# Kernel optimization log

Measured on AMD Instinct MI355X. Metric: run time of the kernel, lower is better.

The kernel has to match this reference:

```python
import jax, jax.numpy as jnp
import numpy as np

B, N, D = 32, 2048, 1024


def setup_inputs() -> dict:
    key = jax.random.key(0)
    k1, k2, k3, k4, k5, k6 = jax.random.split(key, 6)
    encoded = jax.random.normal(k1, (B, N, D), dtype=jnp.float32)
    decoder_state = jax.random.normal(k2, (B, D), dtype=jnp.float32)
    mask = jax.random.randint(k3, (B, N), 0, 2, dtype=jnp.int32)
    scale = 1.0 / np.sqrt(D)
    W1 = jax.random.normal(k4, (D, D), dtype=jnp.float32) * scale  # applied as x @ W1
    W2 = jax.random.normal(k5, (D, D), dtype=jnp.float32) * scale
    vt = jax.random.normal(k6, (D,), dtype=jnp.float32) * scale
    return {"encoded": encoded, "decoder_state": decoder_state, "mask": mask,
            "W1": W1, "W2": W2, "vt": vt}


def reference(encoded, decoder_state, mask, W1, W2, vt):
    temperature = 1.0
    # process_encoded: W1(encoded)  [B, N, D]
    enc = jnp.einsum('bnd,de->bne', encoded, W1)
    # W2(decoder_state)  [B, D] -> broadcast-add over N
    dec = decoder_state @ W2
    # vt(tanh(.)).squeeze(2)  -> logits [B, N]
    u = jnp.einsum('bnd,d->bn', jnp.tanh(enc + dec[:, None, :]), vt)
    # masked log-softmax with temperature over dim=1
    logits = u / temperature + jnp.log(mask.astype(u.dtype) + 1e-45)
    return jax.nn.log_softmax(logits, axis=1)
```

## Files before the change

### kernel.cpp

```cpp
#include <hip/hip_runtime.h>

typedef _Float16 half8 __attribute__((ext_vector_type(8)));
typedef __fp16   pk2   __attribute__((ext_vector_type(2)));
typedef float    f32x4 __attribute__((ext_vector_type(4)));

#define GLOBAL_AS __attribute__((address_space(1)))
#define LDS_AS    __attribute__((address_space(3)))

static constexpr int Bb = 32;
static constexpr int Nn = 2048;
static constexpr int Dd = 1024;
static constexpr int M  = Bb * Nn;


__global__ void prep_w1(const float* __restrict__ W1, _Float16* __restrict__ W1TT) {
    int g = blockIdx.x * 256 + threadIdx.x;
    int chunk = g >> 10;
    int u = g & 1023;
    int q = u >> 7, sc = u & 127;
    int cl = sc ^ (2 * (q & 3));
    int et = chunk >> 5, t = (chunk >> 1) & 15, h = chunk & 1;
    int e  = et * 256 + h * 128 + cl;
    int k0 = t * 64 + q * 8;
    half8 hh;
#pragma unroll
    for (int j = 0; j < 8; ++j)
        hh[j] = (_Float16)W1[(size_t)(k0 + j) * Dd + e];
    *(half8*)(W1TT + (size_t)g * 8) = hh;
}

__global__ void prep_enc(const float* __restrict__ A, _Float16* __restrict__ A_p) {
    __shared__ _Float16 T[128 * 64];
    const int c = blockIdx.x;
    const int tid = threadIdx.x;
    const int mtile = c >> 5, t = (c >> 1) & 15, h = c & 1;
    const int r = tid >> 1, kh = tid & 1;
    const float* src = A + (size_t)(mtile * 256 + h * 128 + r) * Dd + t * 64 + kh * 32;
    const int rx = r & 7;
#pragma unroll
    for (int i = 0; i < 4; ++i) {
        f32x4 a  = *(const f32x4*)(src + i * 8);
        f32x4 b2 = *(const f32x4*)(src + i * 8 + 4);
        half8 hh; pk2 p;
        p = __builtin_amdgcn_cvt_pkrtz(a.x, a.y);   hh[0] = p[0]; hh[1] = p[1];
        p = __builtin_amdgcn_cvt_pkrtz(a.z, a.w);   hh[2] = p[0]; hh[3] = p[1];
        p = __builtin_amdgcn_cvt_pkrtz(b2.x, b2.y); hh[4] = p[0]; hh[5] = p[1];
        p = __builtin_amdgcn_cvt_pkrtz(b2.z, b2.w); hh[6] = p[0]; hh[7] = p[1];
        *(half8*)(T + r * 64 + (((kh * 4 + i) ^ rx) * 8)) = hh;
    }
    __syncthreads();
    const size_t cb = (size_t)c * 8192;
#pragma unroll
    for (int i = 0; i < 4; ++i) {
        int u = i * 256 + tid;
        int q = u >> 7, sr = u & 127;
        int lr = sr ^ (2 * (q & 3));
        half8 hh = *(const half8*)(T + lr * 64 + ((q ^ (lr & 7)) * 8));
        *(half8*)(A_p + cb + (size_t)u * 8) = hh;
    }
}

__global__ void dec_kernel(const float* __restrict__ ds, const float* __restrict__ W2,
                           float* __restrict__ dec) {
    __shared__ float part[4][64];
    int b = blockIdx.x, ech = blockIdx.y;
    int tid = threadIdx.x;
    int e = ech * 64 + (tid & 63);
    int dc = tid >> 6;
    float acc = 0.f;
#pragma unroll 4
    for (int d = dc * 256; d < dc * 256 + 256; ++d)
        acc += ds[b * Dd + d] * W2[(size_t)d * Dd + e];
    part[dc][tid & 63] = acc;
    __syncthreads();
    if (tid < 64)
        dec[b * Dd + e] = part[0][tid] + part[1][tid] + part[2][tid] + part[3][tid];
}

#define BAR     asm volatile("s_barrier" ::: "memory")
#define LGKM(n) asm volatile("s_waitcnt lgkmcnt(" #n ")" ::: "memory")
#define VM(n)   asm volatile("s_waitcnt vmcnt(" #n ")" ::: "memory")

#define RD_A(dst, base) do { _Pragma("unroll") \
  for (int ks = 0; ks < 2; ++ks) { const int qb = ((ks * 4 + qq) * 128) * 8; \
    _Pragma("unroll") for (int m2 = 0; m2 < 4; ++m2) \
      dst[m2][ks] = *(const half8*)&lds[(base) + qb + (m2 * 32 + rA) * 8]; } } while (0)

#define RD_B(dst, base) do { _Pragma("unroll") \
  for (int ks = 0; ks < 2; ++ks) { const int qb = ((ks * 4 + qq) * 128) * 8; \
    _Pragma("unroll") for (int j2 = 0; j2 < 2; ++j2) \
      dst[j2][ks] = *(const half8*)&lds[(base) + qb + (j2 * 64 + rB) * 8]; } } while (0)

#define MFMAQ(A_, B_, ro, co) do { __builtin_amdgcn_s_setprio(1); \
  _Pragma("unroll") for (int m2 = 0; m2 < 4; ++m2) \
  _Pragma("unroll") for (int j2 = 0; j2 < 2; ++j2) { \
    acc[(ro) + m2][(co) + j2] = __builtin_amdgcn_mfma_f32_16x16x32_f16( \
        A_[m2][0], B_[j2][0], acc[(ro) + m2][(co) + j2], 0, 0, 0); \
    acc[(ro) + m2][(co) + j2] = __builtin_amdgcn_mfma_f32_16x16x32_f16( \
        A_[m2][1], B_[j2][1], acc[(ro) + m2][(co) + j2], 0, 0, 0); } \
  __builtin_amdgcn_s_setprio(0); } while (0)

__global__ __launch_bounds__(512) void gemm8(
    const _Float16* __restrict__ A_p, const _Float16* __restrict__ W1TT,
    const float* __restrict__ dec, const float* __restrict__ vt,
    float* __restrict__ u_part)
{
    extern __shared__ _Float16 lds[];

    const int g  = blockIdx.x;
    const int wg = (g & 7) * 128 + (g >> 3);
    const int et    = wg & 3;
    const int mtile = wg >> 2;

    const int tid  = threadIdx.x;
    const int lane = tid & 63, wid = tid >> 6;
    const int wr = wid >> 2, wc = wid & 3;
    const int qq = lane >> 4, l15 = lane & 15;
    const int l15s = l15 ^ (2 * qq);
    const int rA = wr * 16 + l15s;
    const int rB = wc * 16 + l15s;

    f32x4 acc[8][4] = {};
    half8 a0[4][2], a1[4][2], b0[2][2], b1[2][2];

    const size_t abase = (size_t)mtile * 32 * 8192;
    const size_t bbase = (size_t)et * 32 * 8192;
    const int uoff = tid * 8;

    auto stA = [&](int t2, int h) {
        const _Float16* gp = A_p + abase + ((size_t)(t2 * 2 + h) << 13) + uoff;
        _Float16* lp = lds + ((((t2 & 1) * 2 + h) << 13) + (wid << 9));
        __builtin_amdgcn_global_load_lds((const GLOBAL_AS void*)gp,
                                         (LDS_AS void*)lp, 16, 0, 0);
        __builtin_amdgcn_global_load_lds((const GLOBAL_AS void*)(gp + 4096),
                                         (LDS_AS void*)(lp + 4096), 16, 0, 0);
    };
    auto stB = [&](int t2, int h) {
        const _Float16* gp = W1TT + bbase + ((size_t)(t2 * 2 + h) << 13) + uoff;
        _Float16* lp = lds + (32768 + (((t2 & 1) * 2 + h) << 13) + (wid << 9));
        __builtin_amdgcn_global_load_lds((const GLOBAL_AS void*)gp,
                                         (LDS_AS void*)lp, 16, 0, 0);
        __builtin_amdgcn_global_load_lds((const GLOBAL_AS void*)(gp + 4096),
                                         (LDS_AS void*)(lp + 4096), 16, 0, 0);
    };

    stA(0, 0); stB(0, 1); stA(0, 1); stB(0, 0); stA(1, 0); stB(1, 1);
    VM(4);
    BAR;
    RD_A(a0, 0);
    RD_B(b0, 32768);

#pragma unroll 1
    for (int i = 0; i < 8; ++i) {
        const int E = 2 * i, O = E + 1;
        const bool nl = (i < 7);

        RD_B(b1, 32768 + 8192);
        stA(O, 1);
        BAR; LGKM(4);
        MFMAQ(a0, b0, 0, 0);
        BAR;

        RD_A(a1, 8192);
        stB(O, 0);
        BAR; LGKM(8);
        MFMAQ(a0, b1, 0, 2);
        VM(6);
        BAR;

        RD_A(a0, 16384);
        if (nl) stA(E + 2, 0);
        BAR; LGKM(8);
        MFMAQ(a1, b1, 4, 2);
        BAR;

        if (nl) { stB(E + 2, 1); VM(4); }
        else    { VM(0); }
        BAR;
        MFMAQ(a1, b0, 4, 0);
        RD_B(b0, 32768 + 16384);
        BAR;

        RD_B(b1, 32768 + 16384 + 8192);
        if (nl) stA(E + 2, 1);
        BAR; LGKM(4);
        MFMAQ(a0, b0, 0, 0);
        BAR;

        RD_A(a1, 16384 + 8192);
        if (nl) stB(E + 2, 0);
        BAR; LGKM(8);
        MFMAQ(a0, b1, 0, 2);
        VM(6);
        BAR;

        if (nl) { RD_A(a0, 0);
                  stA(O + 2, 0); }
        BAR;
        if (nl) { LGKM(8); } else { LGKM(0); }
        MFMAQ(a1, b1, 4, 2);
        BAR;

        if (nl) stB(O + 2, 1);
        VM(4);
        BAR;
        MFMAQ(a1, b0, 4, 0);
        if (nl) RD_B(b0, 32768);
        BAR;
    }

    const int b = mtile >> 3;
    float vtv[4], dcv[4];
#pragma unroll
    for (int nf = 0; nf < 4; ++nf) {
        int e = et * 256 + (nf >> 1) * 128 + (nf & 1) * 64 + wc * 16 + l15;
        vtv[nf] = vt[e];
        dcv[nf] = dec[b * Dd + e];
    }
    float* usum = (float*)lds;
#pragma unroll
    for (int hm = 0; hm < 8; ++hm) {
        const int h = hm >> 2, m = hm & 3;
#pragma unroll
        for (int r = 0; r < 4; ++r) {
            float s = 0.f;
#pragma unroll
            for (int nf = 0; nf < 4; ++nf) {
                float x  = acc[hm][nf][r] + dcv[nf];
                float ex = __expf(2.f * x);
                s += (1.f - 2.f * __builtin_amdgcn_rcpf(ex + 1.f)) * vtv[nf];
            }
#pragma unroll
            for (int off = 1; off < 16; off <<= 1) s += __shfl_xor(s, off, 16);
            if (l15 == 0)
                usum[wc * 256 + h * 128 + m * 32 + wr * 16 + qq * 4 + r] = s;
        }
    }
    __syncthreads();
    if (tid < 256) {
        float v = usum[tid] + usum[256 + tid] + usum[512 + tid] + usum[768 + tid];
        u_part[(size_t)et * M + (size_t)mtile * 256 + tid] = v;
    }
}

__global__ void softmax_k(const float* __restrict__ up, const int* __restrict__ mask,
                          float* __restrict__ out) {
    __shared__ float red[8];
    int b = blockIdx.x, tid = threadIdx.x;
    float l[8];
#pragma unroll
    for (int i = 0; i < 8; ++i) {
        int n = i * 256 + tid;
        float s = up[(size_t)b * Nn + n];
#pragma unroll
        for (int et = 1; et < 4; ++et) s += up[(size_t)et * M + (size_t)b * Nn + n];
        l[i] = s + (mask[b * Nn + n] ? 0.f : -103.278931f);
    }
    float m = l[0];
#pragma unroll
    for (int i = 1; i < 8; ++i) m = fmaxf(m, l[i]);
#pragma unroll
    for (int o = 32; o >= 1; o >>= 1) m = fmaxf(m, __shfl_xor(m, o, 64));
    if ((tid & 63) == 0) red[tid >> 6] = m;
    __syncthreads();
    m = fmaxf(fmaxf(red[0], red[1]), fmaxf(red[2], red[3]));
    float s = 0.f;
#pragma unroll
    for (int i = 0; i < 8; ++i) s += expf(l[i] - m);
#pragma unroll
    for (int o = 32; o >= 1; o >>= 1) s += __shfl_xor(s, o, 64);
    if ((tid & 63) == 0) red[4 + (tid >> 6)] = s;
    __syncthreads();
    float lse = m + logf(red[4] + red[5] + red[6] + red[7]);
#pragma unroll
    for (int i = 0; i < 8; ++i)
        out[(size_t)b * Nn + i * 256 + tid] = l[i] - lse;
}

extern "C" void kernel_launch(void* const* d_in, const int* in_sizes, int n_in,
                              void* d_out, int out_size, void* d_ws, size_t ws_size,
                              hipStream_t stream) {
    const float* encoded = (const float*)d_in[0];
    const float* dstate  = (const float*)d_in[1];
    const int*   mask    = (const int*)d_in[2];
    const float* W1      = (const float*)d_in[3];
    const float* W2      = (const float*)d_in[4];
    const float* vt      = (const float*)d_in[5];
    float* out = (float*)d_out;

    char* ws = (char*)d_ws;
    float*    u_part = (float*)ws;
    float*    dec    = (float*)(ws + (size_t)4 * M * 4);
    _Float16* W1TT   = (_Float16*)(ws + (size_t)4 * M * 4 + (size_t)Bb * Dd * 4);
    _Float16* A_p    = (_Float16*)(ws + (size_t)4 * M * 4 + (size_t)Bb * Dd * 4
                                   + (size_t)Dd * Dd * 2);

    static bool attr_done = false;
    if (!attr_done) {
        hipFuncSetAttribute(reinterpret_cast<const void*>(gemm8),
                            hipFuncAttributeMaxDynamicSharedMemorySize, 131072);
        attr_done = true;
    }

    prep_w1<<<512, 256, 0, stream>>>(W1, W1TT);
    dec_kernel<<<dim3(32, 16), 256, 0, stream>>>(dstate, W2, dec);
    prep_enc<<<8192, 256, 0, stream>>>(encoded, A_p);
    gemm8<<<1024, 512, 131072, stream>>>(A_p, W1TT, dec, vt, u_part);
    softmax_k<<<32, 256, 0, stream>>>(u_part, mask, out);
}
```

Before: 574.9 us.

## Process two M-tiles per GEMM workgroup with continuous prefetch across tiles

Each workgroup now computes two consecutive 256-row M-tiles in one 16-iteration K loop, with the B-operand index wrapping so loads for the next tile are prefetched during the current tile's epilogue. This halves the grid and removes the per-tile pipeline fill and drain. The LDS reduction across the four column waves is dropped; each wave writes its partial logits directly to a 16-way u_part buffer, and the softmax kernel sums all 16 partials. The cost is more global partial traffic, a larger workspace, and the epilogue tanh work running inside the main loop.

Result: slower. 663.2 us (+15.3%).

```diff
diff --git a/kernel.cpp b/kernel.cpp
--- a/kernel.cpp
+++ b/kernel.cpp
@@ -108,9 +108,10 @@
     extern __shared__ _Float16 lds[];
 
     const int g  = blockIdx.x;
-    const int wg = (g & 7) * 128 + (g >> 3);
-    const int et    = wg & 3;
-    const int mtile = wg >> 2;
+    const int wg = (g & 7) * 64 + (g >> 3);
+    const int et   = wg & 3;
+    const int mgrp = wg >> 2;
+    const int m0 = mgrp * 2;
 
     const int tid  = threadIdx.x;
     const int lane = tid & 63, wid = tid >> 6;
@@ -123,123 +124,130 @@
     f32x4 acc[8][4] = {};
     half8 a0[4][2], a1[4][2], b0[2][2], b1[2][2];
 
-    const size_t abase = (size_t)mtile * 32 * 8192;
+    const int bb = m0 >> 3;
+    float vtv[4], dcv[4];
+#pragma unroll
+    for (int nf = 0; nf < 4; ++nf) {
+        int e = et * 256 + (nf >> 1) * 128 + (nf & 1) * 64 + wc * 16 + l15;
+        vtv[nf] = vt[e];
+        dcv[nf] = dec[bb * Dd + e];
+    }
+
+    const size_t abase = (size_t)m0 * 32 * 8192;
     const size_t bbase = (size_t)et * 32 * 8192;
     const int uoff = tid * 8;
 
-    auto stA = [&](int t2, int h) {
-        const _Float16* gp = A_p + abase + ((size_t)(t2 * 2 + h) << 13) + uoff;
-        _Float16* lp = lds + ((((t2 & 1) * 2 + h) << 13) + (wid << 9));
+    auto stA = [&](int T, int h) {
+        const _Float16* gp = A_p + abase + ((size_t)(2 * T + h) << 13) + uoff;
+        _Float16* lp = lds + ((((T & 1) * 2 + h) << 13) + (wid << 9));
         __builtin_amdgcn_global_load_lds((const GLOBAL_AS void*)gp,
                                          (LDS_AS void*)lp, 16, 0, 0);
         __builtin_amdgcn_global_load_lds((const GLOBAL_AS void*)(gp + 4096),
                                          (LDS_AS void*)(lp + 4096), 16, 0, 0);
     };
-    auto stB = [&](int t2, int h) {
-        const _Float16* gp = W1TT + bbase + ((size_t)(t2 * 2 + h) << 13) + uoff;
-        _Float16* lp = lds + (32768 + (((t2 & 1) * 2 + h) << 13) + (wid << 9));
+    auto stB = [&](int T, int h) {
+        const _Float16* gp = W1TT + bbase + ((size_t)((T & 15) * 2 + h) << 13) + uoff;
+        _Float16* lp = lds + (32768 + (((T & 1) * 2 + h) << 13) + (wid << 9));
         __builtin_amdgcn_global_load_lds((const GLOBAL_AS void*)gp,
                                          (LDS_AS void*)lp, 16, 0, 0);
         __builtin_amdgcn_global_load_lds((const GLOBAL_AS void*)(gp + 4096),
                                          (LDS_AS void*)(lp + 4096), 16, 0, 0);
     };
 
-    stA(0, 0); stB(0, 1); stA(0, 1); stB(0, 0); stA(1, 0); stB(1, 1);
-    VM(4);
+
+    stA(0, 0); stB(0, 0); stB(0, 1); stA(0, 1); stA(1, 0);
+    stB(1, 0); stB(1, 1); stA(1, 1); stA(2, 0);
+    VM(8);
     BAR;
     RD_A(a0, 0);
     RD_B(b0, 32768);
 
 #pragma unroll 1
-    for (int i = 0; i < 8; ++i) {
+    for (int i = 0; i < 16; ++i) {
         const int E = 2 * i, O = E + 1;
-        const bool nl = (i < 7);
+        const bool s1 = (i < 15), s2 = (i < 14);
 
         RD_B(b1, 32768 + 8192);
-        stA(O, 1);
+        if (s1) stB(E + 2, 0);
         BAR; LGKM(4);
         MFMAQ(a0, b0, 0, 0);
         BAR;
 
         RD_A(a1, 8192);
-        stB(O, 0);
+        if (s1) stB(E + 2, 1);
         BAR; LGKM(8);
         MFMAQ(a0, b1, 0, 2);
-        VM(6);
         BAR;
 
         RD_A(a0, 16384);
-        if (nl) stA(E + 2, 0);
+        if (s1) stA(E + 2, 1);
         BAR; LGKM(8);
         MFMAQ(a1, b1, 4, 2);
         BAR;
 
-        if (nl) { stB(E + 2, 1); VM(4); }
-        else    { VM(0); }
+        if (s1) stA(O + 2, 0);
+        if (s1) { VM(8); } else { VM(0); }
         BAR;
         MFMAQ(a1, b0, 4, 0);
         RD_B(b0, 32768 + 16384);
         BAR;
 
         RD_B(b1, 32768 + 16384 + 8192);
-        if (nl) stA(E + 2, 1);
+        if (s1) stB(O + 2, 0);
         BAR; LGKM(4);
         MFMAQ(a0, b0, 0, 0);
         BAR;
 
         RD_A(a1, 16384 + 8192);
-        if (nl) stB(E + 2, 0);
+        if (s1) stB(O + 2, 1);
         BAR; LGKM(8);
         MFMAQ(a0, b1, 0, 2);
-        VM(6);
-        BAR;
-
-        if (nl) { RD_A(a0, 0);
-                  stA(O + 2, 0); }
-        BAR;
-        if (nl) { LGKM(8); } else { LGKM(0); }
+        BAR;
+
+        if (s1) RD_A(a0, 0);
+        if (s1) stA(O + 2, 1);
+        BAR;
+        if (s1) { LGKM(8); } else { LGKM(0); }
         MFMAQ(a1, b1, 4, 2);
         BAR;
 
-        if (nl) stB(O + 2, 1);
-        VM(4);
+        if (s2) stA(E + 4, 0);
+        if (s2)      { VM(8); }
+        else if (s1) { VM(6); }
+        else         { VM(0); }
         BAR;
         MFMAQ(a1, b0, 4, 0);
-        if (nl) RD_B(b0, 32768);
-        BAR;
-    }
-
-    const int b = mtile >> 3;
-    float vtv[4], dcv[4];
-#pragma unroll
-    for (int nf = 0; nf < 4; ++nf) {
-        int e = et * 256 + (nf >> 1) * 128 + (nf & 1) * 64 + wc * 16 + l15;
-        vtv[nf] = vt[e];
-        dcv[nf] = dec[b * Dd + e];
-    }
-    float* usum = (float*)lds;
-#pragma unroll
-    for (int hm = 0; hm < 8; ++hm) {
-        const int h = hm >> 2, m = hm & 3;
-#pragma unroll
-        for (int r = 0; r < 4; ++r) {
-            float s = 0.f;
-#pragma unroll
-            for (int nf = 0; nf < 4; ++nf) {
-                float x  = acc[hm][nf][r] + dcv[nf];
-                float ex = __expf(2.f * x);
-                s += (1.f - 2.f * __builtin_amdgcn_rcpf(ex + 1.f)) * vtv[nf];
+        if (s1) RD_B(b0, 32768);
+        BAR;
+
+        if ((i & 7) == 7) {
+            const int mt = m0 + (i >> 3);
+#pragma unroll
+            for (int hm = 0; hm < 8; ++hm) {
+                const int h = hm >> 2, mq = hm & 3;
+#pragma unroll
+                for (int r = 0; r < 4; ++r) {
+                    float s = 0.f;
+#pragma unroll
+                    for (int nf = 0; nf < 4; ++nf) {
+                        float x  = acc[hm][nf][r] + dcv[nf];
+                        float ex = __expf(2.f * x);
+                        s += (1.f - 2.f * __builtin_amdgcn_rcpf(ex + 1.f)) * vtv[nf];
+                    }
+#pragma unroll
+                    for (int off = 1; off < 16; off <<= 1)
+                        s += __shfl_xor(s, off, 16);
+                    if (l15 == 0)
+                        u_part[(size_t)(et * 4 + wc) * M + (size_t)mt * 256
+                               + h * 128 + mq * 32 + wr * 16 + qq * 4 + r] = s;
+                }
             }
 #pragma unroll
-            for (int off = 1; off < 16; off <<= 1) s += __shfl_xor(s, off, 16);
-            if (l15 == 0)
-                usum[wc * 256 + h * 128 + m * 32 + wr * 16 + qq * 4 + r] = s;
+            for (int hm = 0; hm < 8; ++hm)
+#pragma unroll
+                for (int nf = 0; nf < 4; ++nf)
+                    acc[hm][nf] = (f32x4){0.f, 0.f, 0.f, 0.f};
         }
-    }
-    __syncthreads();
-    if (tid < 256) {
-        float v = usum[tid] + usum[256 + tid] + usum[512 + tid] + usum[768 + tid];
-        u_part[(size_t)et * M + (size_t)mtile * 256 + tid] = v;
     }
 }
 
@@ -253,7 +261,7 @@
         int n = i * 256 + tid;
         float s = up[(size_t)b * Nn + n];
 #pragma unroll
-        for (int et = 1; et < 4; ++et) s += up[(size_t)et * M + (size_t)b * Nn + n];
+        for (int et = 1; et < 16; ++et) s += up[(size_t)et * M + (size_t)b * Nn + n];
         l[i] = s + (mask[b * Nn + n] ? 0.f : -103.278931f);
     }
     float m = l[0];
@@ -290,9 +298,9 @@
 
     char* ws = (char*)d_ws;
     float*    u_part = (float*)ws;
-    float*    dec    = (float*)(ws + (size_t)4 * M * 4);
-    _Float16* W1TT   = (_Float16*)(ws + (size_t)4 * M * 4 + (size_t)Bb * Dd * 4);
-    _Float16* A_p    = (_Float16*)(ws + (size_t)4 * M * 4 + (size_t)Bb * Dd * 4
+    float*    dec    = (float*)(ws + (size_t)16 * M * 4);
+    _Float16* W1TT   = (_Float16*)(ws + (size_t)16 * M * 4 + (size_t)Bb * Dd * 4);
+    _Float16* A_p    = (_Float16*)(ws + (size_t)16 * M * 4 + (size_t)Bb * Dd * 4
                                    + (size_t)Dd * Dd * 2);
 
     static bool attr_done = false;
@@ -305,6 +313,6 @@
     prep_w1<<<512, 256, 0, stream>>>(W1, W1TT);
     dec_kernel<<<dim3(32, 16), 256, 0, stream>>>(dstate, W2, dec);
     prep_enc<<<8192, 256, 0, stream>>>(encoded, A_p);
-    gemm8<<<1024, 512, 131072, stream>>>(A_p, W1TT, dec, vt, u_part);
+    gemm8<<<512, 512, 131072, stream>>>(A_p, W1TT, dec, vt, u_part);
     softmax_k<<<32, 256, 0, stream>>>(u_part, mask, out);
 }
```

## Restructure GEMM main loop into four phases with a single A register buffer

Applied to the files above, without the earlier changes.

Replaces the eight-phase, double-register-buffered main loop of the fp16 MFMA GEMM with a four-phase schedule. Each phase reads one A half-tile into a single register set, reuses both B fragments for 16 MFMAs, and issues the global-to-LDS prefetch for the next tile with simpler vmcnt waits. Setprio now wraps a larger MFMA group instead of each quarter. Dropping the second A register buffer cuts register pressure, but waiting on lgkmcnt(0) before each MFMA group exposes more LDS read latency.

Measured after the change: 565.6 us. No clear change (-1.6%).

```diff
diff --git a/kernel.cpp b/kernel.cpp
--- a/kernel.cpp
+++ b/kernel.cpp
@@ -80,6 +80,8 @@
 #define BAR     asm volatile("s_barrier" ::: "memory")
 #define LGKM(n) asm volatile("s_waitcnt lgkmcnt(" #n ")" ::: "memory")
 #define VM(n)   asm volatile("s_waitcnt vmcnt(" #n ")" ::: "memory")
+#define PRIO1   __builtin_amdgcn_s_setprio(1)
+#define PRIO0   __builtin_amdgcn_s_setprio(0)
 
 #define RD_A(dst, base) do { _Pragma("unroll") \
   for (int ks = 0; ks < 2; ++ks) { const int qb = ((ks * 4 + qq) * 128) * 8; \
@@ -91,14 +93,13 @@
     _Pragma("unroll") for (int j2 = 0; j2 < 2; ++j2) \
       dst[j2][ks] = *(const half8*)&lds[(base) + qb + (j2 * 64 + rB) * 8]; } } while (0)
 
-#define MFMAQ(A_, B_, ro, co) do { __builtin_amdgcn_s_setprio(1); \
+#define MFMAQ(A_, B_, ro, co) do { \
   _Pragma("unroll") for (int m2 = 0; m2 < 4; ++m2) \
   _Pragma("unroll") for (int j2 = 0; j2 < 2; ++j2) { \
     acc[(ro) + m2][(co) + j2] = __builtin_amdgcn_mfma_f32_16x16x32_f16( \
         A_[m2][0], B_[j2][0], acc[(ro) + m2][(co) + j2], 0, 0, 0); \
     acc[(ro) + m2][(co) + j2] = __builtin_amdgcn_mfma_f32_16x16x32_f16( \
-        A_[m2][1], B_[j2][1], acc[(ro) + m2][(co) + j2], 0, 0, 0); } \
-  __builtin_amdgcn_s_setprio(0); } while (0)
+        A_[m2][1], B_[j2][1], acc[(ro) + m2][(co) + j2], 0, 0, 0); } } while (0)
 
 __global__ __launch_bounds__(512) void gemm8(
     const _Float16* __restrict__ A_p, const _Float16* __restrict__ W1TT,
@@ -121,91 +122,69 @@
     const int rB = wc * 16 + l15s;
 
     f32x4 acc[8][4] = {};
-    half8 a0[4][2], a1[4][2], b0[2][2], b1[2][2];
+    half8 a[4][2], b0[2][2], b1[2][2];
 
     const size_t abase = (size_t)mtile * 32 * 8192;
     const size_t bbase = (size_t)et * 32 * 8192;
     const int uoff = tid * 8;
 
-    auto stA = [&](int t2, int h) {
-        const _Float16* gp = A_p + abase + ((size_t)(t2 * 2 + h) << 13) + uoff;
-        _Float16* lp = lds + ((((t2 & 1) * 2 + h) << 13) + (wid << 9));
+    auto stA = [&](int T, int h) {
+        const _Float16* gp = A_p + abase + ((size_t)(T * 2 + h) << 13) + uoff;
+        _Float16* lp = lds + ((((T & 1) * 2 + h) << 13) + (wid << 9));
         __builtin_amdgcn_global_load_lds((const GLOBAL_AS void*)gp,
                                          (LDS_AS void*)lp, 16, 0, 0);
         __builtin_amdgcn_global_load_lds((const GLOBAL_AS void*)(gp + 4096),
                                          (LDS_AS void*)(lp + 4096), 16, 0, 0);
     };
-    auto stB = [&](int t2, int h) {
-        const _Float16* gp = W1TT + bbase + ((size_t)(t2 * 2 + h) << 13) + uoff;
-        _Float16* lp = lds + (32768 + (((t2 & 1) * 2 + h) << 13) + (wid << 9));
+    auto stB = [&](int T, int h) {
+        const _Float16* gp = W1TT + bbase + ((size_t)(T * 2 + h) << 13) + uoff;
+        _Float16* lp = lds + (32768 + (((T & 1) * 2 + h) << 13) + (wid << 9));
         __builtin_amdgcn_global_load_lds((const GLOBAL_AS void*)gp,
                                          (LDS_AS void*)lp, 16, 0, 0);
         __builtin_amdgcn_global_load_lds((const GLOBAL_AS void*)(gp + 4096),
                                          (LDS_AS void*)(lp + 4096), 16, 0, 0);
     };
 
-    stA(0, 0); stB(0, 1); stA(0, 1); stB(0, 0); stA(1, 0); stB(1, 1);
-    VM(4);
+
+    stA(0, 0); stB(0, 0); stB(0, 1); stA(0, 1);
+    VM(2);
     BAR;
-    RD_A(a0, 0);
-    RD_B(b0, 32768);
 
 #pragma unroll 1
     for (int i = 0; i < 8; ++i) {
         const int E = 2 * i, O = E + 1;
-        const bool nl = (i < 7);
-
-        RD_B(b1, 32768 + 8192);
+        const bool s = (i < 7);
+
+        RD_A(a, 0);
+        RD_B(b0, 32768);
+        RD_B(b1, 40960);
+        stA(O, 0); stB(O, 0); stB(O, 1);
+        BAR; LGKM(0);
+        PRIO1; MFMAQ(a, b0, 0, 0); MFMAQ(a, b1, 0, 2); PRIO0;
+        VM(6);
+        BAR;
+
+        RD_A(a, 8192);
         stA(O, 1);
-        BAR; LGKM(4);
-        MFMAQ(a0, b0, 0, 0);
-        BAR;
-
-        RD_A(a1, 8192);
-        stB(O, 0);
-        BAR; LGKM(8);
-        MFMAQ(a0, b1, 0, 2);
-        VM(6);
-        BAR;
-
-        RD_A(a0, 16384);
-        if (nl) stA(E + 2, 0);
-        BAR; LGKM(8);
-        MFMAQ(a1, b1, 4, 2);
-        BAR;
-
-        if (nl) { stB(E + 2, 1); VM(4); }
-        else    { VM(0); }
-        BAR;
-        MFMAQ(a1, b0, 4, 0);
-        RD_B(b0, 32768 + 16384);
-        BAR;
-
-        RD_B(b1, 32768 + 16384 + 8192);
-        if (nl) stA(E + 2, 1);
-        BAR; LGKM(4);
-        MFMAQ(a0, b0, 0, 0);
-        BAR;
-
-        RD_A(a1, 16384 + 8192);
-        if (nl) stB(E + 2, 0);
-        BAR; LGKM(8);
-        MFMAQ(a0, b1, 0, 2);
-        VM(6);
-        BAR;
-
-        if (nl) { RD_A(a0, 0);
-                  stA(O + 2, 0); }
-        BAR;
-        if (nl) { LGKM(8); } else { LGKM(0); }
-        MFMAQ(a1, b1, 4, 2);
-        BAR;
-
-        if (nl) stB(O + 2, 1);
-        VM(4);
-        BAR;
-        MFMAQ(a1, b0, 4, 0);
-        if (nl) RD_B(b0, 32768);
+        BAR; LGKM(0);
+        PRIO1; MFMAQ(a, b0, 4, 0); MFMAQ(a, b1, 4, 2); PRIO0;
+        VM(2);
+        BAR;
+
+        RD_A(a, 16384);
+        RD_B(b0, 49152);
+        RD_B(b1, 57344);
+        if (s) { stA(E + 2, 0); stB(E + 2, 0); stB(E + 2, 1); }
+        BAR; LGKM(0);
+        PRIO1; MFMAQ(a, b0, 0, 0); MFMAQ(a, b1, 0, 2); PRIO0;
+        if (s) { VM(6); } else { VM(0); }
+        BAR;
+
+        RD_A(a, 24576);
+        if (s) stA(E + 2, 1);
+        BAR; LGKM(0);
+        PRIO1; MFMAQ(a, b0, 4, 0); MFMAQ(a, b1, 4, 2); PRIO0;
+        VM(2);
         BAR;
     }
 
@@ -220,20 +199,20 @@
     float* usum = (float*)lds;
 #pragma unroll
     for (int hm = 0; hm < 8; ++hm) {
-        const int h = hm >> 2, m = hm & 3;
+        const int h = hm >> 2, mq = hm & 3;
 #pragma unroll
         for (int r = 0; r < 4; ++r) {
-            float s = 0.f;
+            float sv = 0.f;
 #pragma unroll
             for (int nf = 0; nf < 4; ++nf) {
                 float x  = acc[hm][nf][r] + dcv[nf];
                 float ex = __expf(2.f * x);
-                s += (1.f - 2.f * __builtin_amdgcn_rcpf(ex + 1.f)) * vtv[nf];
+                sv += (1.f - 2.f * __builtin_amdgcn_rcpf(ex + 1.f)) * vtv[nf];
             }
 #pragma unroll
-            for (int off = 1; off < 16; off <<= 1) s += __shfl_xor(s, off, 16);
+            for (int off = 1; off < 16; off <<= 1) sv += __shfl_xor(sv, off, 16);
             if (l15 == 0)
-                usum[wc * 256 + h * 128 + m * 32 + wr * 16 + qq * 4 + r] = s;
+                usum[wc * 256 + h * 128 + mq * 32 + wr * 16 + qq * 4 + r] = sv;
         }
     }
     __syncthreads();
```
